# Optimization experiments

Measured on AMD Instinct MI355X. Metric: run time of the kernel, lower is better.

The kernel has to match this reference:

```python
import jax, jax.numpy as jnp
import numpy as np

H = 128  # hidden_size


def _run_lstm(x, Wx, Wh, b):
    """Unidirectional LSTM over x:(B,T,F). Returns (hs:(B,T,H), c_final:(B,H)).
    Matches flax nn.LSTMCell: gates [i,f,g,o]; input dense has no bias,
    hidden dense has bias b; carry=(c,h), carry[0]=c."""
    B, T, _ = x.shape
    # Hoist the input projection out of the scan: one big GEMM.
    xp = jnp.einsum('btf,fg->tbg', x, Wx) + b  # (T,B,4H)

    def step(carry, gx):
        c, h = carry
        g = gx + h @ Wh  # (B,4H)
        i = jax.nn.sigmoid(g[:, :H])
        f = jax.nn.sigmoid(g[:, H:2 * H])
        gg = jnp.tanh(g[:, 2 * H:3 * H])
        o = jax.nn.sigmoid(g[:, 3 * H:])
        c_new = f * c + i * gg
        h_new = o * jnp.tanh(c_new)
        return (c_new, h_new), h_new

    init = (jnp.zeros((B, H), x.dtype), jnp.zeros((B, H), x.dtype))
    (c_fin, _h_fin), hs = jax.lax.scan(step, init, xp)
    return jnp.swapaxes(hs, 0, 1), c_fin


def _forward(x, params):
    # params: list of (Wx_f, Wh_f, b_f, Wx_b, Wh_b, b_b) per layer
    for li, (Wxf, Whf, bf, Wxb, Whb, bb) in enumerate(params):
        out_f, c_f = _run_lstm(x, Wxf, Whf, bf)
        out_b_rev, c_b = _run_lstm(jnp.flip(x, axis=1), Wxb, Whb, bb)
        out_b = jnp.flip(out_b_rev, axis=1)
        x = jnp.concatenate([out_f, out_b], axis=-1)
        # dropout is identity in eval mode (deterministic reference)
    # NOTE: original code takes carry[0], which in flax LSTMCell is the CELL state.
    h_final = jnp.concatenate([c_f, c_b], axis=-1)
    return x, h_final


def setup_inputs() -> dict:
    key = jax.random.key(0)
    ks = jax.random.split(key, 16)
    B, T, F = 32, 2048, 128
    d = {'x': jax.random.normal(ks[0], (B, T, F), jnp.float32)}
    shapes = {
        'Wx_f0': (F, 4 * H), 'Wh_f0': (H, 4 * H),
        'Wx_b0': (F, 4 * H), 'Wh_b0': (H, 4 * H),
        'Wx_f1': (2 * H, 4 * H), 'Wh_f1': (H, 4 * H),
        'Wx_b1': (2 * H, 4 * H), 'Wh_b1': (H, 4 * H),
    }
    for i, (name, shp) in enumerate(shapes.items()):
        scale = 1.0 / np.sqrt(shp[0])
        d[name] = jax.random.normal(ks[i + 1], shp, jnp.float32) * scale
    for name in ['b_f0', 'b_b0', 'b_f1', 'b_b1']:
        d[name] = jnp.zeros((4 * H,), jnp.float32)
    return d


def reference(x, Wx_f0, Wh_f0, b_f0, Wx_b0, Wh_b0, b_b0,
              Wx_f1, Wh_f1, b_f1, Wx_b1, Wh_b1, b_b1):
    params = [(Wx_f0, Wh_f0, b_f0, Wx_b0, Wh_b0, b_b0),
              (Wx_f1, Wh_f1, b_f1, Wx_b1, Wh_b1, b_b1)]
    return _forward(x, params)
```

## Files before the change

### kernel.cpp

```cpp
#include <hip/hip_runtime.h>
#include <hip/hip_bf16.h>
#include <stdint.h>
#include <type_traits>


#define DEVINL __device__ __forceinline__

typedef __attribute__((ext_vector_type(8))) short short8;
typedef __attribute__((ext_vector_type(4))) float f32x4;

static constexpr int T = 2048;
static constexpr size_t XOUT = (size_t)32 * T * 256;
static constexpr float L2E = 1.4426950408889634f;
static constexpr float M2L2E = -2.8853900817779268f;

DEVINL unsigned short f2bf(float f) {
  unsigned int u = __float_as_uint(f);
  u += 0x7FFFu + ((u >> 16) & 1u);
  return (unsigned short)(u >> 16);
}
DEVINL float gate_scale(int g) { return (g == 2) ? M2L2E : -L2E; }

__global__ __launch_bounds__(256) void prep_wx(const float* wxf0, const float* wxb0,
                                               const float* wxf1, const float* wxb1,
                                               unsigned short* sw0, unsigned short* sw1) {
  int idx = blockIdx.x * 256 + threadIdx.x;
  if (idx < 2 * 65536) {
    int d = idx >> 16;
    int local = idx & 65535;
    const float* w = d ? wxb0 : wxf0;
    int e = local & 7, lane = (local >> 3) & 63, ks = (local >> 9) & 3, ng = local >> 11;
    int col = ng * 16 + (lane & 15);
    int k = ks * 32 + ((lane >> 4) << 3) + e;
    sw0[idx] = f2bf(w[k * 512 + col] * gate_scale(ng >> 3));
  } else {
    int j = idx - 2 * 65536;
    if (j < 2 * 131072) {
      int d = j >> 17;
      int local = j & 131071;
      const float* w = d ? wxb1 : wxf1;
      int e = local & 7, lane = (local >> 3) & 63, ks = (local >> 9) & 7, ng = local >> 12;
      int col = ng * 16 + (lane & 15);
      int k = ks * 32 + ((lane >> 4) << 3) + e;
      sw1[j] = f2bf(w[k * 512 + col] * gate_scale(ng >> 3));
    }
  }
}

__global__ __launch_bounds__(256) void prep_wh(const float* whf0, const float* whb0,
                                               const float* whf1, const float* whb1,
                                               unsigned short* swh) {
  int idx = blockIdx.x * 256 + threadIdx.x;
  if (idx >= 262144) return;
  int e = idx & 7, lane = (idx >> 3) & 63, wid = (idx >> 9) & 7;
  int ks = (idx >> 12) & 3, g = (idx >> 14) & 3, dir = (idx >> 16) & 1, layer = (idx >> 17) & 1;
  const float* w = layer ? (dir ? whb1 : whf1) : (dir ? whb0 : whf0);
  int col = g * 128 + wid * 16 + (lane & 15);
  int k = ks * 32 + ((lane >> 4) << 3) + e;
  swh[idx] = f2bf(w[k * 512 + col] * gate_scale(g));
}

template <int LAYER, bool XPF32>
__global__ __launch_bounds__(256) void input_proj(const float* x, const unsigned short* a_bf,
                                                  const unsigned short* wsw,
                                                  const float* bias_f, const float* bias_b,
                                                  void* xp_out) {
  constexpr int KS = (LAYER == 0) ? 4 : 8;
  int t = blockIdx.x, dir = blockIdx.y;
  int wid = threadIdx.x >> 6, lane = threadIdx.x & 63;
  int p = lane >> 4, c15 = lane & 15;
  const unsigned short* wbase = wsw + (size_t)dir * (32 * KS * 64 * 8);
  const float* bias = dir ? bias_b : bias_f;

  short8 afrag[2][KS];
#pragma unroll
  for (int mt = 0; mt < 2; ++mt) {
#pragma unroll
    for (int ks = 0; ks < KS; ++ks) {
      int m = c15 + mt * 16;
      int kk = ks * 32 + (p << 3);
      if constexpr (LAYER == 0) {
        const float* ap = x + (size_t)m * (T * 128) + (size_t)t * 128 + kk;
        float4 lov = *(const float4*)ap;
        float4 hiv = *(const float4*)(ap + 4);
        short8 s;
        s[0] = (short)f2bf(lov.x); s[1] = (short)f2bf(lov.y);
        s[2] = (short)f2bf(lov.z); s[3] = (short)f2bf(lov.w);
        s[4] = (short)f2bf(hiv.x); s[5] = (short)f2bf(hiv.y);
        s[6] = (short)f2bf(hiv.z); s[7] = (short)f2bf(hiv.w);
        afrag[mt][ks] = s;
      } else {
        afrag[mt][ks] = *(const short8*)(a_bf + ((size_t)t * 32 + m) * 256 + kk);
      }
    }
  }

#pragma unroll
  for (int ngi = 0; ngi < 8; ++ngi) {
    int ng = wid * 8 + ngi;
    int g = ng >> 3, wd = ng & 7;
    f32x4 acc0 = {0.f, 0.f, 0.f, 0.f};
    f32x4 acc1 = {0.f, 0.f, 0.f, 0.f};
#pragma unroll
    for (int ks = 0; ks < KS; ++ks) {
      short8 b = *(const short8*)(wbase + ((size_t)(ng * KS + ks) * 64 + lane) * 8);
      acc0 = __builtin_amdgcn_mfma_f32_16x16x32_bf16(afrag[0][ks], b, acc0, 0, 0, 0);
      acc1 = __builtin_amdgcn_mfma_f32_16x16x32_bf16(afrag[1][ks], b, acc1, 0, 0, 0);
    }
    float bs = bias[ng * 16 + c15] * gate_scale(g);
    int gcol = wd * 16 + c15;
#pragma unroll
    for (int mt = 0; mt < 2; ++mt) {
      f32x4 v = (mt == 0) ? acc0 : acc1;
      v[0] += bs; v[1] += bs; v[2] += bs; v[3] += bs;
      size_t base = (size_t)t * 16384 + (size_t)((mt * 4 + p) * 2048 + gcol * 4 + g);
      if constexpr (XPF32) {
        float* xpf = (float*)xp_out + (size_t)dir * ((size_t)T * 16384);
#pragma unroll
        for (int r = 0; r < 4; ++r) xpf[base + r * 512] = v[r];
      } else {
        unsigned short* xpb = (unsigned short*)xp_out + (size_t)dir * ((size_t)T * 16384);
#pragma unroll
        for (int r = 0; r < 4; ++r) xpb[base + r * 512] = f2bf(v[r]);
      }
    }
  }
}

DEVINL f32x4 gx2v(float4 v) { f32x4 r; r[0]=v.x; r[1]=v.y; r[2]=v.z; r[3]=v.w; return r; }
DEVINL f32x4 gx2v(uint2 u) {
  f32x4 r;
  r[0] = __uint_as_float(u.x << 16);
  r[1] = __uint_as_float(u.x & 0xFFFF0000u);
  r[2] = __uint_as_float(u.y << 16);
  r[3] = __uint_as_float(u.y & 0xFFFF0000u);
  return r;
}
DEVINL float sel4(f32x4 a, int p) {
  float s01 = (p & 1) ? a[1] : a[0];
  float s23 = (p & 1) ? a[3] : a[2];
  return (p & 2) ? s23 : s01;
}
DEVINL float actstep(float pi, float pf, float pg, float po, float& c) {
  float ei = __builtin_amdgcn_exp2f(pi);
  float ef = __builtin_amdgcn_exp2f(pf);
  float eg = __builtin_amdgcn_exp2f(pg);
  float eo = __builtin_amdgcn_exp2f(po);
  float ai = 1.0f + ei, av = 1.0f + ef, ag = 1.0f + eg, sg = 1.0f - eg;
  float pp = ai * ag;
  float num = __builtin_fmaf(c, pp, sg * av);
  float rd = __builtin_amdgcn_rcpf(av * pp);
  float cn = num * rd;
  c = cn;
  float ec = __builtin_amdgcn_exp2f(M2L2E * cn);
  float ao = 1.0f + eo, ac = 1.0f + ec, sc = 1.0f - ec;
  float rd2 = __builtin_amdgcn_rcpf(ao * ac);
  return sc * rd2;
}

template <int LAYER, bool XPF32>
__global__ __launch_bounds__(512) void lstm_scan(const void* xp, const unsigned short* swh,
                                                 unsigned short* out0, float* dout) {
  using gxT = typename std::conditional<XPF32, float4, uint2>::type;
  int dir = blockIdx.x >> 3;
  int q = blockIdx.x & 7;
  int wid = threadIdx.x >> 6, lane = threadIdx.x & 63;
  int c15 = lane & 15, p = lane >> 4;
  int col = wid * 16 + c15;

  __shared__ __align__(16) unsigned char hA[1280];
  __shared__ __align__(16) unsigned char hB[1280];

  const unsigned short* whbase = swh + (size_t)LAYER * 131072 + (size_t)dir * 65536;
  short8 whf[4][4];
#pragma unroll
  for (int g = 0; g < 4; ++g)
#pragma unroll
    for (int ks = 0; ks < 4; ++ks)
      whf[g][ks] = *(const short8*)(whbase + g * 16384 + ks * 4096 + wid * 512 + lane * 8);

  if (threadIdx.x < 288) {
    ((unsigned int*)hA)[threadIdx.x] = 0u;
    ((unsigned int*)hB)[threadIdx.x] = 0u;
  }

  int aoff[4];
#pragma unroll
  for (int ks = 0; ks < 4; ++ks)
    aoff[ks] = (lane & 3) * 288 + ((lane >> 4) << 4) + ks * 64;
  int woff = p * 288 + col * 2;

  const gxT* xpg = (const gxT*)xp + (size_t)dir * ((size_t)T * 4096);
  int og = q * 512 + p * 128 + col;

  int b = q * 4 + p;
  float cs = 0.f;

  int t0 = dir ? (T - 1) : 0;
  int ts = dir ? -1 : 1;

  const gxT* gxp = xpg + (size_t)t0 * 4096;
  unsigned short* outp = out0 + (size_t)t0 * 8192 + b * 256 + dir * 128 + col;
  float* dp = dout + ((size_t)b * T + t0) * 256 + dir * 128 + col;
  const ptrdiff_t GXS = (ptrdiff_t)ts * 4096;
  const ptrdiff_t OUS = (ptrdiff_t)ts * 8192;
  const ptrdiff_t DPS = (ptrdiff_t)ts * 256;

  gxT ga = gxp[og];
  gxT gb;
  __syncthreads();

#define STEP(RD, WR, GC, GN)                                                       \
  {                                                                                \
    short8 af0 = *(const short8*)((const char*)(RD) + aoff[0]);                    \
    short8 af1 = *(const short8*)((const char*)(RD) + aoff[1]);                    \
    short8 af2 = *(const short8*)((const char*)(RD) + aoff[2]);                    \
    short8 af3 = *(const short8*)((const char*)(RD) + aoff[3]);                    \
    const f32x4 zz = {0.f, 0.f, 0.f, 0.f};                                         \
    f32x4 acc0 = __builtin_amdgcn_mfma_f32_16x16x32_bf16(af0, whf[0][0], zz, 0, 0, 0); \
    f32x4 acc1 = __builtin_amdgcn_mfma_f32_16x16x32_bf16(af0, whf[1][0], zz, 0, 0, 0); \
    f32x4 acc2 = __builtin_amdgcn_mfma_f32_16x16x32_bf16(af0, whf[2][0], zz, 0, 0, 0); \
    f32x4 acc3 = __builtin_amdgcn_mfma_f32_16x16x32_bf16(af0, whf[3][0], zz, 0, 0, 0); \
    gxp += GXS;                                                                    \
    GN = gxp[og];                                                                  \
    acc0 = __builtin_amdgcn_mfma_f32_16x16x32_bf16(af1, whf[0][1], acc0, 0, 0, 0); \
    acc1 = __builtin_amdgcn_mfma_f32_16x16x32_bf16(af1, whf[1][1], acc1, 0, 0, 0); \
    acc2 = __builtin_amdgcn_mfma_f32_16x16x32_bf16(af1, whf[2][1], acc2, 0, 0, 0); \
    acc3 = __builtin_amdgcn_mfma_f32_16x16x32_bf16(af1, whf[3][1], acc3, 0, 0, 0); \
    acc0 = __builtin_amdgcn_mfma_f32_16x16x32_bf16(af2, whf[0][2], acc0, 0, 0, 0); \
    acc1 = __builtin_amdgcn_mfma_f32_16x16x32_bf16(af2, whf[1][2], acc1, 0, 0, 0); \
    acc2 = __builtin_amdgcn_mfma_f32_16x16x32_bf16(af2, whf[2][2], acc2, 0, 0, 0); \
    acc3 = __builtin_amdgcn_mfma_f32_16x16x32_bf16(af2, whf[3][2], acc3, 0, 0, 0); \
    acc0 = __builtin_amdgcn_mfma_f32_16x16x32_bf16(af3, whf[0][3], acc0, 0, 0, 0); \
    acc1 = __builtin_amdgcn_mfma_f32_16x16x32_bf16(af3, whf[1][3], acc1, 0, 0, 0); \
    acc2 = __builtin_amdgcn_mfma_f32_16x16x32_bf16(af3, whf[2][3], acc2, 0, 0, 0); \
    acc3 = __builtin_amdgcn_mfma_f32_16x16x32_bf16(af3, whf[3][3], acc3, 0, 0, 0); \
    f32x4 gv = gx2v(GC);                                                           \
    float pi = sel4(acc0, p) + gv[0];                                              \
    float pf = sel4(acc1, p) + gv[1];                                              \
    float pg = sel4(acc2, p) + gv[2];                                              \
    float po = sel4(acc3, p) + gv[3];                                              \
    float hv = actstep(pi, pf, pg, po, cs);                                        \
    unsigned int pk;                                                               \
    asm("v_cvt_pk_bf16_f32 %0, %1, %2" : "=v"(pk) : "v"(hv), "v"(hv));             \
    unsigned short hb = (unsigned short)pk;                                        \
    *(unsigned short*)((char*)(WR) + woff) = hb;                                   \
    if (LAYER == 0) {                                                              \
      *outp = hb;                                                                  \
      outp += OUS;                                                                 \
    } else {                                                                       \
      *dp = hv;                                                                    \
      dp += DPS;                                                                   \
    }                                                                              \
    asm volatile("s_waitcnt lgkmcnt(0)" ::: "memory");                             \
    __builtin_amdgcn_s_barrier();                                                  \
    asm volatile("" ::: "memory");                                                 \
  }

  for (int s = 0; s < T; s += 2) {
    STEP(hA, hB, ga, gb);
    STEP(hB, hA, gb, ga);
  }
#undef STEP

  if constexpr (LAYER == 1) {
    dout[XOUT + (size_t)b * 256 + dir * 128 + col] = cs;
  }
}

extern "C" void kernel_launch(void* const* d_in, const int* in_sizes, int n_in,
                              void* d_out, int out_size, void* d_ws, size_t ws_size,
                              hipStream_t stream) {
  const float* x    = (const float*)d_in[0];
  const float* wxf0 = (const float*)d_in[1];
  const float* whf0 = (const float*)d_in[2];
  const float* wxb0 = (const float*)d_in[3];
  const float* whb0 = (const float*)d_in[4];
  const float* wxf1 = (const float*)d_in[5];
  const float* whf1 = (const float*)d_in[6];
  const float* wxb1 = (const float*)d_in[7];
  const float* whb1 = (const float*)d_in[8];
  const float* bf0  = (const float*)d_in[9];
  const float* bb0  = (const float*)d_in[10];
  const float* bf1  = (const float*)d_in[11];
  const float* bb1  = (const float*)d_in[12];
  float* dout = (float*)d_out;

  const size_t needF32 = 268435456u + 33554432u + 262144u + 524288u + 524288u;
  bool xpf32 = ws_size >= needF32;
  size_t xpBytes = xpf32 ? 268435456u : 134217728u;
  unsigned char* ws = (unsigned char*)d_ws;
  void* xp = (void*)ws;
  unsigned short* out0 = (unsigned short*)(ws + xpBytes);
  unsigned short* sw0  = (unsigned short*)(ws + xpBytes + 33554432u);
  unsigned short* sw1  = sw0 + 2 * 65536;
  unsigned short* swh  = sw1 + 2 * 131072;

  prep_wx<<<1536, 256, 0, stream>>>(wxf0, wxb0, wxf1, wxb1, sw0, sw1);
  prep_wh<<<1024, 256, 0, stream>>>(whf0, whb0, whf1, whb1, swh);

  if (xpf32) {
    input_proj<0, true><<<dim3(2048, 2), 256, 0, stream>>>(x, nullptr, sw0, bf0, bb0, xp);
    lstm_scan<0, true><<<16, 512, 0, stream>>>(xp, swh, out0, dout);
    input_proj<1, true><<<dim3(2048, 2), 256, 0, stream>>>(nullptr, out0, sw1, bf1, bb1, xp);
    lstm_scan<1, true><<<16, 512, 0, stream>>>(xp, swh, out0, dout);
  } else {
    input_proj<0, false><<<dim3(2048, 2), 256, 0, stream>>>(x, nullptr, sw0, bf0, bb0, xp);
    lstm_scan<0, false><<<16, 512, 0, stream>>>(xp, swh, out0, dout);
    input_proj<1, false><<<dim3(2048, 2), 256, 0, stream>>>(nullptr, out0, sw1, bf1, bb1, xp);
    lstm_scan<1, false><<<16, 512, 0, stream>>>(xp, swh, out0, dout);
  }
}
```

Measured before the change: 1.976 ms.

## Replicate A rows so each lane reads its gate from acc[0], interleave exp with MFMA

Changes the A-fragment LDS offsets so the four batch rows are replicated across the 16 MFMA output rows. Each lane then finds its own batch result in accumulator element 0, which removes the sel4 select chain. Each gate's four MFMAs now run back to back, with that gate's exp2 issued right after, so transcendental work can overlap the remaining matrix ops. The loop is unrolled to four steps, and the output addressing uses a base pointer plus a 32-bit index. The cost is serial accumulator dependency chains within each gate instead of four independent chains interleaved.

```diff
diff --git a/kernel.cpp b/kernel.cpp
--- a/kernel.cpp
+++ b/kernel.cpp
@@ -136,27 +136,6 @@
   r[3] = __uint_as_float(u.y & 0xFFFF0000u);
   return r;
 }
-DEVINL float sel4(f32x4 a, int p) {
-  float s01 = (p & 1) ? a[1] : a[0];
-  float s23 = (p & 1) ? a[3] : a[2];
-  return (p & 2) ? s23 : s01;
-}
-DEVINL float actstep(float pi, float pf, float pg, float po, float& c) {
-  float ei = __builtin_amdgcn_exp2f(pi);
-  float ef = __builtin_amdgcn_exp2f(pf);
-  float eg = __builtin_amdgcn_exp2f(pg);
-  float eo = __builtin_amdgcn_exp2f(po);
-  float ai = 1.0f + ei, av = 1.0f + ef, ag = 1.0f + eg, sg = 1.0f - eg;
-  float pp = ai * ag;
-  float num = __builtin_fmaf(c, pp, sg * av);
-  float rd = __builtin_amdgcn_rcpf(av * pp);
-  float cn = num * rd;
-  c = cn;
-  float ec = __builtin_amdgcn_exp2f(M2L2E * cn);
-  float ao = 1.0f + eo, ac = 1.0f + ec, sc = 1.0f - ec;
-  float rd2 = __builtin_amdgcn_rcpf(ao * ac);
-  return sc * rd2;
-}
 
 template <int LAYER, bool XPF32>
 __global__ __launch_bounds__(512) void lstm_scan(const void* xp, const unsigned short* swh,
@@ -187,10 +166,10 @@
   int aoff[4];
 #pragma unroll
   for (int ks = 0; ks < 4; ++ks)
-    aoff[ks] = (lane & 3) * 288 + ((lane >> 4) << 4) + ks * 64;
+    aoff[ks] = ((lane & 15) >> 2) * 288 + ((lane >> 4) << 4) + ks * 64;
   int woff = p * 288 + col * 2;
 
-  const gxT* xpg = (const gxT*)xp + (size_t)dir * ((size_t)T * 4096);
+  const gxT* gxp = (const gxT*)xp + (size_t)dir * ((size_t)T * 4096);
   int og = q * 512 + p * 128 + col;
 
   int b = q * 4 + p;
@@ -199,9 +178,11 @@
   int t0 = dir ? (T - 1) : 0;
   int ts = dir ? -1 : 1;
 
-  const gxT* gxp = xpg + (size_t)t0 * 4096;
-  unsigned short* outp = out0 + (size_t)t0 * 8192 + b * 256 + dir * 128 + col;
-  float* dp = dout + ((size_t)b * T + t0) * 256 + dir * 128 + col;
+  gxp += (size_t)t0 * 4096;
+  unsigned short* outp_u = out0 + (size_t)t0 * 8192;
+  float* dp_u = dout + (size_t)t0 * 256;
+  unsigned int oidx = (unsigned int)(b * 256 + dir * 128 + col);
+  unsigned int didx = (unsigned int)((size_t)b * T * 256 + dir * 128 + col);
   const ptrdiff_t GXS = (ptrdiff_t)ts * 4096;
   const ptrdiff_t OUS = (ptrdiff_t)ts * 8192;
   const ptrdiff_t DPS = (ptrdiff_t)ts * 256;
@@ -217,47 +198,63 @@
     short8 af2 = *(const short8*)((const char*)(RD) + aoff[2]);                    \
     short8 af3 = *(const short8*)((const char*)(RD) + aoff[3]);                    \
     const f32x4 zz = {0.f, 0.f, 0.f, 0.f};                                         \
-    f32x4 acc0 = __builtin_amdgcn_mfma_f32_16x16x32_bf16(af0, whf[0][0], zz, 0, 0, 0); \
-    f32x4 acc1 = __builtin_amdgcn_mfma_f32_16x16x32_bf16(af0, whf[1][0], zz, 0, 0, 0); \
-    f32x4 acc2 = __builtin_amdgcn_mfma_f32_16x16x32_bf16(af0, whf[2][0], zz, 0, 0, 0); \
-    f32x4 acc3 = __builtin_amdgcn_mfma_f32_16x16x32_bf16(af0, whf[3][0], zz, 0, 0, 0); \
+    f32x4 gv = gx2v(GC);                                                           \
+                                                                   \
+    f32x4 acc0 = __builtin_amdgcn_mfma_f32_16x16x32_bf16(af0, whf[0][0], zz, 0,0,0); \
+    acc0 = __builtin_amdgcn_mfma_f32_16x16x32_bf16(af1, whf[0][1], acc0, 0, 0, 0); \
+    acc0 = __builtin_amdgcn_mfma_f32_16x16x32_bf16(af2, whf[0][2], acc0, 0, 0, 0); \
+    acc0 = __builtin_amdgcn_mfma_f32_16x16x32_bf16(af3, whf[0][3], acc0, 0, 0, 0); \
+    float ei = __builtin_amdgcn_exp2f(acc0[0] + gv[0]);                            \
+                                                                   \
+    f32x4 acc1 = __builtin_amdgcn_mfma_f32_16x16x32_bf16(af0, whf[1][0], zz, 0,0,0); \
+    acc1 = __builtin_amdgcn_mfma_f32_16x16x32_bf16(af1, whf[1][1], acc1, 0, 0, 0); \
+    acc1 = __builtin_amdgcn_mfma_f32_16x16x32_bf16(af2, whf[1][2], acc1, 0, 0, 0); \
+    acc1 = __builtin_amdgcn_mfma_f32_16x16x32_bf16(af3, whf[1][3], acc1, 0, 0, 0); \
+    float ef = __builtin_amdgcn_exp2f(acc1[0] + gv[1]);                            \
     gxp += GXS;                                                                    \
     GN = gxp[og];                                                                  \
-    acc0 = __builtin_amdgcn_mfma_f32_16x16x32_bf16(af1, whf[0][1], acc0, 0, 0, 0); \
-    acc1 = __builtin_amdgcn_mfma_f32_16x16x32_bf16(af1, whf[1][1], acc1, 0, 0, 0); \
+                                                                   \
+    f32x4 acc2 = __builtin_amdgcn_mfma_f32_16x16x32_bf16(af0, whf[2][0], zz, 0,0,0); \
     acc2 = __builtin_amdgcn_mfma_f32_16x16x32_bf16(af1, whf[2][1], acc2, 0, 0, 0); \
+    acc2 = __builtin_amdgcn_mfma_f32_16x16x32_bf16(af2, whf[2][2], acc2, 0, 0, 0); \
+    acc2 = __builtin_amdgcn_mfma_f32_16x16x32_bf16(af3, whf[2][3], acc2, 0, 0, 0); \
+    float eg = __builtin_amdgcn_exp2f(acc2[0] + gv[2]);                            \
+                                                                   \
+    f32x4 acc3 = __builtin_amdgcn_mfma_f32_16x16x32_bf16(af0, whf[3][0], zz, 0,0,0); \
     acc3 = __builtin_amdgcn_mfma_f32_16x16x32_bf16(af1, whf[3][1], acc3, 0, 0, 0); \
-    acc0 = __builtin_amdgcn_mfma_f32_16x16x32_bf16(af2, whf[0][2], acc0, 0, 0, 0); \
-    acc1 = __builtin_amdgcn_mfma_f32_16x16x32_bf16(af2, whf[1][2], acc1, 0, 0, 0); \
-    acc2 = __builtin_amdgcn_mfma_f32_16x16x32_bf16(af2, whf[2][2], acc2, 0, 0, 0); \
     acc3 = __builtin_amdgcn_mfma_f32_16x16x32_bf16(af2, whf[3][2], acc3, 0, 0, 0); \
-    acc0 = __builtin_amdgcn_mfma_f32_16x16x32_bf16(af3, whf[0][3], acc0, 0, 0, 0); \
-    acc1 = __builtin_amdgcn_mfma_f32_16x16x32_bf16(af3, whf[1][3], acc1, 0, 0, 0); \
-    acc2 = __builtin_amdgcn_mfma_f32_16x16x32_bf16(af3, whf[2][3], acc2, 0, 0, 0); \
     acc3 = __builtin_amdgcn_mfma_f32_16x16x32_bf16(af3, whf[3][3], acc3, 0, 0, 0); \
-    f32x4 gv = gx2v(GC);                                                           \
-    float pi = sel4(acc0, p) + gv[0];                                              \
-    float pf = sel4(acc1, p) + gv[1];                                              \
-    float pg = sel4(acc2, p) + gv[2];                                              \
-    float po = sel4(acc3, p) + gv[3];                                              \
-    float hv = actstep(pi, pf, pg, po, cs);                                        \
+    float eo = __builtin_amdgcn_exp2f(acc3[0] + gv[3]);                            \
+                               \
+    float ai = 1.0f + ei, av = 1.0f + ef, ag = 1.0f + eg, sg = 1.0f - eg;          \
+    float pp = ai * ag;                                                            \
+    float num = __builtin_fmaf(cs, pp, sg * av);                                   \
+    float rd = __builtin_amdgcn_rcpf(av * pp);                                     \
+    float cn = num * rd;                                                           \
+    cs = cn;                                                                       \
+    float ec = __builtin_amdgcn_exp2f(M2L2E * cn);                                 \
+    float ao = 1.0f + eo, ac = 1.0f + ec, sc = 1.0f - ec;                          \
+    float rd2 = __builtin_amdgcn_rcpf(ao * ac);                                    \
+    float hv = sc * rd2;                                                           \
     unsigned int pk;                                                               \
     asm("v_cvt_pk_bf16_f32 %0, %1, %2" : "=v"(pk) : "v"(hv), "v"(hv));             \
     unsigned short hb = (unsigned short)pk;                                        \
     *(unsigned short*)((char*)(WR) + woff) = hb;                                   \
     if (LAYER == 0) {                                                              \
-      *outp = hb;                                                                  \
-      outp += OUS;                                                                 \
+      outp_u[oidx] = hb;                                                           \
+      outp_u += OUS;                                                               \
     } else {                                                                       \
-      *dp = hv;                                                                    \
-      dp += DPS;                                                                   \
+      dp_u[didx] = hv;                                                             \
+      dp_u += DPS;                                                                 \
     }                                                                              \
     asm volatile("s_waitcnt lgkmcnt(0)" ::: "memory");                             \
     __builtin_amdgcn_s_barrier();                                                  \
     asm volatile("" ::: "memory");                                                 \
   }
 
-  for (int s = 0; s < T; s += 2) {
+  for (int s = 0; s < T; s += 4) {
+    STEP(hA, hB, ga, gb);
+    STEP(hB, hA, gb, ga);
     STEP(hA, hB, ga, gb);
     STEP(hB, hA, gb, ga);
   }
```

Measured after the change: 1.781 ms, median of 2. 9.9% less time.
